# Kernel tuning notes

Measured on AMD Instinct MI355X. Metric: run time of the kernel, lower is better.

Reference implementation:

```python
import jax, jax.numpy as jnp
import numpy as np

ALPHA = 20.0 / 100.0  # dt / tau
NOISE_SCALE = 0.1 * (2.0 * ALPHA) ** 0.5  # network_noise * sqrt(2*alpha)

T, B, I, H, O = 512, 64, 128, 512, 64


def setup_inputs() -> dict:
    key = jax.random.key(0)
    ks = jax.random.split(key, 6)
    s_in = 1.0 / np.sqrt(I)
    s_h = 1.0 / np.sqrt(H)
    return {
        "x": jax.random.normal(ks[0], (T, B, I), jnp.float32),
        "noise": jax.random.normal(ks[1], (T, B, H), jnp.float32),
        "W_in": jax.random.normal(ks[2], (H, I), jnp.float32) * s_in,
        "W_rec": jax.random.normal(ks[3], (H, H), jnp.float32) * s_h,
        "b_rec": jnp.zeros((H,), jnp.float32),
        "W_out": jax.random.normal(ks[4], (O, H), jnp.float32) * s_h,
        "b_out": jnp.zeros((O,), jnp.float32),
    }


def reference(x, noise, W_in, W_rec, b_rec, W_out, b_out):
    # Precompute input projection for all timesteps: (T, B, H)
    xin = jnp.einsum("tbi,hi->tbh", x, W_in)

    def step(hidden, inp):
        xin_t, noise_t = inp
        h_new = jax.nn.relu(xin_t + hidden @ W_rec.T + b_rec)
        h_new = hidden * (1.0 - ALPHA) + h_new * ALPHA
        h_new = h_new + noise_t * NOISE_SCALE
        return h_new, h_new

    h0 = jnp.zeros((x.shape[1], W_rec.shape[0]), x.dtype)
    _, rnn_output = jax.lax.scan(step, h0, (xin, noise))  # (T, B, H)
    output = jnp.einsum("tbh,oh->tbo", rnn_output, W_out) + b_out
    return output, rnn_output
```

## Files before the change

### kernel.cpp

```cpp
#include <hip/hip_runtime.h>

constexpr int T  = 512;
constexpr int NB = 64;
constexpr int NI = 128;
constexpr int NH = 512;
constexpr int NO = 64;

constexpr float ALPHA = 0.2f;
constexpr float NSC   = 0.063245553203367586f;

typedef _Float16 h2_t __attribute__((ext_vector_type(2)));

#if defined(__has_builtin)
#  if __has_builtin(__builtin_amdgcn_fdot2)
#    define HAS_FDOT2 1
#  endif
#endif
#ifndef HAS_FDOT2
#  define HAS_FDOT2 0
#endif

__device__ __forceinline__ float dot2(uint32_t wbits, uint32_t hbits, float acc) {
#if HAS_FDOT2
    return __builtin_amdgcn_fdot2(__builtin_bit_cast(h2_t, wbits),
                                  __builtin_bit_cast(h2_t, hbits), acc, false);
#else
    const h2_t wv = __builtin_bit_cast(h2_t, wbits);
    const h2_t hv = __builtin_bit_cast(h2_t, hbits);
    return acc + (float)wv.x * (float)hv.x + (float)wv.y * (float)hv.y;
#endif
}

__device__ __forceinline__ uint32_t pk2(float x, float y) {
    return __builtin_bit_cast(uint32_t, (h2_t){(_Float16)x, (_Float16)y});
}

__global__ __launch_bounds__(256) void k_gemm_nt_bias(
    const float* __restrict__ A, const float* __restrict__ Bm,
    const float* __restrict__ bias, float* __restrict__ C,
    int M, int N, int K)
{
    __shared__ __align__(16) float As[32][68];
    __shared__ __align__(16) float Bs[32][68];
    const int tid = threadIdx.x;
    const int tx = tid & 15, ty = tid >> 4;
    const long row0 = (long)blockIdx.x * 64;
    const long col0 = (long)blockIdx.y * 64;
    const int lr = tid >> 3;
    const int lq = tid & 7;

    float acc[4][4] = {};

    for (int kt = 0; kt < K; kt += 32) {
        #pragma unroll
        for (int hh = 0; hh < 2; ++hh) {
            const int r = lr + hh * 32;
            const float4 va = *(const float4*)&A[(size_t)(row0 + r) * K + kt + lq * 4];
            As[lq*4+0][r] = va.x; As[lq*4+1][r] = va.y;
            As[lq*4+2][r] = va.z; As[lq*4+3][r] = va.w;
            const float4 vb = *(const float4*)&Bm[(size_t)(col0 + r) * K + kt + lq * 4];
            Bs[lq*4+0][r] = vb.x; Bs[lq*4+1][r] = vb.y;
            Bs[lq*4+2][r] = vb.z; Bs[lq*4+3][r] = vb.w;
        }
        __syncthreads();
        #pragma unroll
        for (int kk = 0; kk < 32; ++kk) {
            const float4 a4 = *(const float4*)&As[kk][ty * 4];
            const float4 b4 = *(const float4*)&Bs[kk][tx * 4];
            const float a[4] = {a4.x, a4.y, a4.z, a4.w};
            const float b[4] = {b4.x, b4.y, b4.z, b4.w};
            #pragma unroll
            for (int i = 0; i < 4; ++i)
                #pragma unroll
                for (int j = 0; j < 4; ++j)
                    acc[i][j] += a[i] * b[j];
        }
        __syncthreads();
    }

    #pragma unroll
    for (int i = 0; i < 4; ++i) {
        const long r = row0 + ty * 4 + i;
        const int  cc = (int)col0 + tx * 4;
        float4 ov;
        ov.x = acc[i][0] + bias[cc + 0];
        ov.y = acc[i][1] + bias[cc + 1];
        ov.z = acc[i][2] + bias[cc + 2];
        ov.w = acc[i][3] + bias[cc + 3];
        *(float4*)&C[(size_t)r * N + cc] = ov;
    }
}

__device__ __forceinline__ uint32_t pack_h(float h, uint32_t tag) {
    const _Float16 hf = (_Float16)h;
    const uint32_t hb = __builtin_bit_cast(unsigned short, hf);
    return (hb << 16) | (tag & 0xFFFFu);
}

__global__ __launch_bounds__(512, 2) void k_rnn(
    const float* __restrict__ W_rec,
    const float* __restrict__ noise,
    float* __restrict__ rnn,
    uint32_t* __restrict__ ex)
{
    const int bid = blockIdx.x;
    const int g = bid & 63;
    const int m = bid >> 6;
    const int tid = threadIdx.x;
    const int w = tid >> 6;
    const int l = tid & 63;

    __shared__ __align__(16) unsigned short hbf[NH];
    __shared__ __align__(16) float pr[8][128];

    uint32_t wa0,wa1,wa2,wa3,wa4,wa5,wa6,wa7,wa8,wa9,wa10,wa11,wa12,wa13,wa14,wa15,
             wa16,wa17,wa18,wa19,wa20,wa21,wa22,wa23,wa24,wa25,wa26,wa27,wa28,wa29,wa30,wa31;
    uint32_t wb0,wb1,wb2,wb3,wb4,wb5,wb6,wb7,wb8,wb9,wb10,wb11,wb12,wb13,wb14,wb15,
             wb16,wb17,wb18,wb19,wb20,wb21,wb22,wb23,wb24,wb25,wb26,wb27,wb28,wb29,wb30,wb31;
    {
        const float* p0 = W_rec + (size_t)(m * 128 + l) * NH + w * 64;
        const float* p1 = W_rec + (size_t)(m * 128 + l + 64) * NH + w * 64;
#define LDW(P, VA, VB, OFF) { const float4 q_ = *(const float4*)((P) + (OFF)); \
                              VA = pk2(q_.x, q_.y); VB = pk2(q_.z, q_.w); }
        LDW(p0, wa0,  wa1,   0) LDW(p0, wa2,  wa3,   4)
        LDW(p0, wa4,  wa5,   8) LDW(p0, wa6,  wa7,  12)
        LDW(p0, wa8,  wa9,  16) LDW(p0, wa10, wa11, 20)
        LDW(p0, wa12, wa13, 24) LDW(p0, wa14, wa15, 28)
        LDW(p0, wa16, wa17, 32) LDW(p0, wa18, wa19, 36)
        LDW(p0, wa20, wa21, 40) LDW(p0, wa22, wa23, 44)
        LDW(p0, wa24, wa25, 48) LDW(p0, wa26, wa27, 52)
        LDW(p0, wa28, wa29, 56) LDW(p0, wa30, wa31, 60)
        LDW(p1, wb0,  wb1,   0) LDW(p1, wb2,  wb3,   4)
        LDW(p1, wb4,  wb5,   8) LDW(p1, wb6,  wb7,  12)
        LDW(p1, wb8,  wb9,  16) LDW(p1, wb10, wb11, 20)
        LDW(p1, wb12, wb13, 24) LDW(p1, wb14, wb15, 28)
        LDW(p1, wb16, wb17, 32) LDW(p1, wb18, wb19, 36)
        LDW(p1, wb20, wb21, 40) LDW(p1, wb22, wb23, 44)
        LDW(p1, wb24, wb25, 48) LDW(p1, wb26, wb27, 52)
        LDW(p1, wb28, wb29, 56) LDW(p1, wb30, wb31, 60)
#undef LDW
    }
#define PIN8(A,B,C,D,E,F,G,H) asm volatile("" : "+v"(A),"+v"(B),"+v"(C),"+v"(D),"+v"(E),"+v"(F),"+v"(G),"+v"(H));
    PIN8(wa0,wa1,wa2,wa3,wa4,wa5,wa6,wa7)
    PIN8(wa8,wa9,wa10,wa11,wa12,wa13,wa14,wa15)
    PIN8(wa16,wa17,wa18,wa19,wa20,wa21,wa22,wa23)
    PIN8(wa24,wa25,wa26,wa27,wa28,wa29,wa30,wa31)
    PIN8(wb0,wb1,wb2,wb3,wb4,wb5,wb6,wb7)
    PIN8(wb8,wb9,wb10,wb11,wb12,wb13,wb14,wb15)
    PIN8(wb16,wb17,wb18,wb19,wb20,wb21,wb22,wb23)
    PIN8(wb24,wb25,wb26,wb27,wb28,wb29,wb30,wb31)
#undef PIN8

    const int gc = m * 128 + tid;

    const int q    = tid - 128;
    const int pp   = q >> 7;
    const int pm   = pp + (pp >= m ? 1 : 0);
    const int pcol = pm * 128 + (q & 127);

    hbf[tid] = 0;

    float hreg = 0.f;

    float xin_pf = 0.f, noi_pf = 0.f;
    if (tid < 128) {
        xin_pf = rnn[(size_t)g * NH + gc];
        noi_pf = noise[(size_t)g * NH + gc];
    }
    __syncthreads();

    int alive  = 1;
    int budget = 1 << 16;

    for (int t = 0; t < T; ++t) {
        float aA0 = 0.f, aA1 = 0.f, aB0 = 0.f, aB1 = 0.f;
        {
            const uint4* hp = (const uint4*)&hbf[w * 64];
#define DOTB(N, A0, A1, A2, A3) { const uint4 u_ = hp[N]; \
            aA0 = dot2(wa##A0, u_.x, aA0); aA1 = dot2(wa##A1, u_.y, aA1); \
            aA0 = dot2(wa##A2, u_.z, aA0); aA1 = dot2(wa##A3, u_.w, aA1); \
            aB0 = dot2(wb##A0, u_.x, aB0); aB1 = dot2(wb##A1, u_.y, aB1); \
            aB0 = dot2(wb##A2, u_.z, aB0); aB1 = dot2(wb##A3, u_.w, aB1); }
            DOTB(0,  0,  1,  2,  3)
            DOTB(1,  4,  5,  6,  7)
            DOTB(2,  8,  9, 10, 11)
            DOTB(3, 12, 13, 14, 15)
            DOTB(4, 16, 17, 18, 19)
            DOTB(5, 20, 21, 22, 23)
            DOTB(6, 24, 25, 26, 27)
            DOTB(7, 28, 29, 30, 31)
#undef DOTB
        }
        pr[w][l]      = aA0 + aA1;
        pr[w][l + 64] = aB0 + aB1;
        __syncthreads();

        const uint32_t want = (uint32_t)(t + 1);
        uint32_t* slot = ex + (size_t)(t & 1) * NB * NH;

        if (tid < 128) {
            float sum = 0.f;
            #pragma unroll
            for (int k = 0; k < 8; ++k) sum += pr[k][tid];
            const float hn = fmaxf(xin_pf + sum, 0.f);
            const float nw = (1.f - ALPHA) * hreg + ALPHA * hn + NSC * noi_pf;
            hreg = nw;
            const uint32_t pk = pack_h(nw, want);
            (void)__hip_atomic_exchange(&slot[(size_t)g * NH + gc], pk,
                                        __ATOMIC_RELAXED, __HIP_MEMORY_SCOPE_AGENT);
            hbf[gc] = (unsigned short)(pk >> 16);
            rnn[((size_t)t * NB + g) * NH + gc] = nw;
            const int tn = (t + 1 < T) ? (t + 1) : t;
            xin_pf = rnn[((size_t)tn * NB + g) * NH + gc];
            noi_pf = noise[((size_t)tn * NB + g) * NH + gc];
        } else {
            uint32_t v;
            if (alive) {
                for (;;) {
                    v = __hip_atomic_fetch_or(&slot[(size_t)g * NH + pcol], 0u,
                                              __ATOMIC_RELAXED, __HIP_MEMORY_SCOPE_AGENT);
                    if ((v & 0xFFFFu) == (want & 0xFFFFu)) break;
                    __builtin_amdgcn_s_sleep(1);
                    if (--budget < 0) { alive = 0; break; }
                }
            } else {
                v = __hip_atomic_fetch_or(&slot[(size_t)g * NH + pcol], 0u,
                                          __ATOMIC_RELAXED, __HIP_MEMORY_SCOPE_AGENT);
            }
            hbf[pcol] = (unsigned short)(v >> 16);
        }
        __syncthreads();
    }
}

extern "C" void kernel_launch(void* const* d_in, const int* in_sizes, int n_in,
                              void* d_out, int out_size, void* d_ws, size_t ws_size,
                              hipStream_t stream)
{
    (void)in_sizes; (void)n_in; (void)out_size; (void)ws_size;
    const float* x     = (const float*)d_in[0];
    const float* noise = (const float*)d_in[1];
    const float* W_in  = (const float*)d_in[2];
    const float* W_rec = (const float*)d_in[3];
    const float* b_rec = (const float*)d_in[4];
    const float* W_out = (const float*)d_in[5];
    const float* b_out = (const float*)d_in[6];

    float* out = (float*)d_out;
    float* rnn = out + (size_t)T * NB * NO;

    uint32_t* ex = (uint32_t*)d_ws;

    hipMemsetAsync(ex, 0, (size_t)2 * NB * NH * sizeof(uint32_t), stream);

    hipLaunchKernelGGL(k_gemm_nt_bias, dim3((T * NB) / 64, NH / 64), dim3(256), 0, stream,
                       x, W_in, b_rec, rnn, T * NB, NH, NI);

    hipLaunchKernelGGL(k_rnn, dim3(256), dim3(512), 0, stream,
                       W_rec, noise, rnn, ex);

    hipLaunchKernelGGL(k_gemm_nt_bias, dim3((T * NB) / 64, NO / 64), dim3(256), 0, stream,
                       rnn, W_out, b_out, out, T * NB, NO, NH);
}
```

Measured before the change: 734.3 us.

## Process two batch rows per RNN block and enlarge GEMM tiles

The recurrent kernel now assigns two batch rows to each workgroup, reusing the register-resident W_rec slice for both. This halves the number of workgroups (128 instead of 256) and the cross-block exchange traffic per row pair, at the cost of double polling and more LDS per block. The projection GEMMs move to templated 128-row tiles with larger per-thread accumulators for better reuse. The inline-asm register pinning of the weights is removed, which may change register allocation.

Result: slower. 1.141 ms (+55.4%).

```diff
diff --git a/kernel.cpp b/kernel.cpp
--- a/kernel.cpp
+++ b/kernel.cpp
@@ -35,59 +35,68 @@
     return __builtin_bit_cast(uint32_t, (h2_t){(_Float16)x, (_Float16)y});
 }
 
-__global__ __launch_bounds__(256) void k_gemm_nt_bias(
+template<int TN>
+__global__ __launch_bounds__(256) void k_gemm_t(
     const float* __restrict__ A, const float* __restrict__ Bm,
     const float* __restrict__ bias, float* __restrict__ C,
     int M, int N, int K)
 {
-    __shared__ __align__(16) float As[32][68];
-    __shared__ __align__(16) float Bs[32][68];
+    constexpr int NA = TN / 16;
+    __shared__ __align__(16) float As[16][132];
+    __shared__ __align__(16) float Bs[16][TN + 4];
     const int tid = threadIdx.x;
     const int tx = tid & 15, ty = tid >> 4;
-    const long row0 = (long)blockIdx.x * 64;
-    const long col0 = (long)blockIdx.y * 64;
-    const int lr = tid >> 3;
-    const int lq = tid & 7;
-
-    float acc[4][4] = {};
-
-    for (int kt = 0; kt < K; kt += 32) {
-        #pragma unroll
-        for (int hh = 0; hh < 2; ++hh) {
-            const int r = lr + hh * 32;
-            const float4 va = *(const float4*)&A[(size_t)(row0 + r) * K + kt + lq * 4];
-            As[lq*4+0][r] = va.x; As[lq*4+1][r] = va.y;
-            As[lq*4+2][r] = va.z; As[lq*4+3][r] = va.w;
-            const float4 vb = *(const float4*)&Bm[(size_t)(col0 + r) * K + kt + lq * 4];
-            Bs[lq*4+0][r] = vb.x; Bs[lq*4+1][r] = vb.y;
-            Bs[lq*4+2][r] = vb.z; Bs[lq*4+3][r] = vb.w;
-        }
-        __syncthreads();
-        #pragma unroll
-        for (int kk = 0; kk < 32; ++kk) {
-            const float4 a4 = *(const float4*)&As[kk][ty * 4];
-            const float4 b4 = *(const float4*)&Bs[kk][tx * 4];
-            const float a[4] = {a4.x, a4.y, a4.z, a4.w};
-            const float b[4] = {b4.x, b4.y, b4.z, b4.w};
+    const long row0 = (long)blockIdx.x * 128;
+    const long col0 = (long)blockIdx.y * TN;
+
+    float acc[8][NA] = {};
+
+    for (int kt = 0; kt < K; kt += 16) {
+        __syncthreads();
+        #pragma unroll
+        for (int f = tid; f < 128 * 4; f += 256) {
+            const int r = f >> 2, ko = (f & 3) * 4;
+            const float4 v = *(const float4*)&A[(row0 + r) * K + kt + ko];
+            As[ko+0][r] = v.x; As[ko+1][r] = v.y;
+            As[ko+2][r] = v.z; As[ko+3][r] = v.w;
+        }
+        #pragma unroll
+        for (int f = tid; f < TN * 4; f += 256) {
+            const int c = f >> 2, ko = (f & 3) * 4;
+            const float4 v = *(const float4*)&Bm[(col0 + c) * K + kt + ko];
+            Bs[ko+0][c] = v.x; Bs[ko+1][c] = v.y;
+            Bs[ko+2][c] = v.z; Bs[ko+3][c] = v.w;
+        }
+        __syncthreads();
+        #pragma unroll
+        for (int kk = 0; kk < 16; ++kk) {
+            float a[8], b[NA];
+            *(float4*)&a[0] = *(const float4*)&As[kk][ty * 8];
+            *(float4*)&a[4] = *(const float4*)&As[kk][ty * 8 + 4];
             #pragma unroll
-            for (int i = 0; i < 4; ++i)
+            for (int j = 0; j < NA; j += 4)
+                *(float4*)&b[j] = *(const float4*)&Bs[kk][tx * NA + j];
+            #pragma unroll
+            for (int i = 0; i < 8; ++i)
                 #pragma unroll
-                for (int j = 0; j < 4; ++j)
+                for (int j = 0; j < NA; ++j)
                     acc[i][j] += a[i] * b[j];
         }
-        __syncthreads();
     }
 
     #pragma unroll
-    for (int i = 0; i < 4; ++i) {
-        const long r = row0 + ty * 4 + i;
-        const int  cc = (int)col0 + tx * 4;
-        float4 ov;
-        ov.x = acc[i][0] + bias[cc + 0];
-        ov.y = acc[i][1] + bias[cc + 1];
-        ov.z = acc[i][2] + bias[cc + 2];
-        ov.w = acc[i][3] + bias[cc + 3];
-        *(float4*)&C[(size_t)r * N + cc] = ov;
+    for (int i = 0; i < 8; ++i) {
+        const long r = row0 + ty * 8 + i;
+        const int cc = (int)col0 + tx * NA;
+        #pragma unroll
+        for (int j = 0; j < NA; j += 4) {
+            float4 ov;
+            ov.x = acc[i][j+0] + bias[cc + j + 0];
+            ov.y = acc[i][j+1] + bias[cc + j + 1];
+            ov.z = acc[i][j+2] + bias[cc + j + 2];
+            ov.w = acc[i][j+3] + bias[cc + j + 3];
+            *(float4*)&C[(size_t)r * N + cc + j] = ov;
+        }
     }
 }
 
@@ -104,14 +113,15 @@
     uint32_t* __restrict__ ex)
 {
     const int bid = blockIdx.x;
-    const int g = bid & 63;
-    const int m = bid >> 6;
+    const int g = bid & 31;
+    const int m = bid >> 5;
     const int tid = threadIdx.x;
     const int w = tid >> 6;
     const int l = tid & 63;
-
-    __shared__ __align__(16) unsigned short hbf[NH];
-    __shared__ __align__(16) float pr[8][128];
+    const int b0 = g * 2, b1 = g * 2 + 1;
+
+    __shared__ __align__(16) unsigned short hbf[2][NH];
+    __shared__ __align__(16) float pr[2][8][128];
 
     uint32_t wa0,wa1,wa2,wa3,wa4,wa5,wa6,wa7,wa8,wa9,wa10,wa11,wa12,wa13,wa14,wa15,
              wa16,wa17,wa18,wa19,wa20,wa21,wa22,wa23,wa24,wa25,wa26,wa27,wa28,wa29,wa30,wa31;
@@ -140,16 +150,6 @@
         LDW(p1, wb28, wb29, 56) LDW(p1, wb30, wb31, 60)
 #undef LDW
     }
-#define PIN8(A,B,C,D,E,F,G,H) asm volatile("" : "+v"(A),"+v"(B),"+v"(C),"+v"(D),"+v"(E),"+v"(F),"+v"(G),"+v"(H));
-    PIN8(wa0,wa1,wa2,wa3,wa4,wa5,wa6,wa7)
-    PIN8(wa8,wa9,wa10,wa11,wa12,wa13,wa14,wa15)
-    PIN8(wa16,wa17,wa18,wa19,wa20,wa21,wa22,wa23)
-    PIN8(wa24,wa25,wa26,wa27,wa28,wa29,wa30,wa31)
-    PIN8(wb0,wb1,wb2,wb3,wb4,wb5,wb6,wb7)
-    PIN8(wb8,wb9,wb10,wb11,wb12,wb13,wb14,wb15)
-    PIN8(wb16,wb17,wb18,wb19,wb20,wb21,wb22,wb23)
-    PIN8(wb24,wb25,wb26,wb27,wb28,wb29,wb30,wb31)
-#undef PIN8
 
     const int gc = m * 128 + tid;
 
@@ -158,14 +158,14 @@
     const int pm   = pp + (pp >= m ? 1 : 0);
     const int pcol = pm * 128 + (q & 127);
 
-    hbf[tid] = 0;
-
-    float hreg = 0.f;
-
-    float xin_pf = 0.f, noi_pf = 0.f;
+    hbf[0][tid] = 0; hbf[1][tid] = 0;
+
+    float hreg0 = 0.f, hreg1 = 0.f;
+
+    float xin0 = 0.f, noi0 = 0.f, xin1 = 0.f, noi1 = 0.f;
     if (tid < 128) {
-        xin_pf = rnn[(size_t)g * NH + gc];
-        noi_pf = noise[(size_t)g * NH + gc];
+        xin0 = rnn[(size_t)b0 * NH + gc];  noi0 = noise[(size_t)b0 * NH + gc];
+        xin1 = rnn[(size_t)b1 * NH + gc];  noi1 = noise[(size_t)b1 * NH + gc];
     }
     __syncthreads();
 
@@ -174,13 +174,19 @@
 
     for (int t = 0; t < T; ++t) {
         float aA0 = 0.f, aA1 = 0.f, aB0 = 0.f, aB1 = 0.f;
+        float cA0 = 0.f, cA1 = 0.f, cB0 = 0.f, cB1 = 0.f;
         {
-            const uint4* hp = (const uint4*)&hbf[w * 64];
-#define DOTB(N, A0, A1, A2, A3) { const uint4 u_ = hp[N]; \
-            aA0 = dot2(wa##A0, u_.x, aA0); aA1 = dot2(wa##A1, u_.y, aA1); \
-            aA0 = dot2(wa##A2, u_.z, aA0); aA1 = dot2(wa##A3, u_.w, aA1); \
-            aB0 = dot2(wb##A0, u_.x, aB0); aB1 = dot2(wb##A1, u_.y, aB1); \
-            aB0 = dot2(wb##A2, u_.z, aB0); aB1 = dot2(wb##A3, u_.w, aB1); }
+            const uint4* hp0 = (const uint4*)&hbf[0][w * 64];
+            const uint4* hp1 = (const uint4*)&hbf[1][w * 64];
+#define DOTB(N, A0, A1, A2, A3) { const uint4 u_ = hp0[N]; const uint4 v_ = hp1[N]; \
+            aA0 = dot2(wa##A0, u_.x, aA0); cA0 = dot2(wa##A0, v_.x, cA0); \
+            aA1 = dot2(wa##A1, u_.y, aA1); cA1 = dot2(wa##A1, v_.y, cA1); \
+            aA0 = dot2(wa##A2, u_.z, aA0); cA0 = dot2(wa##A2, v_.z, cA0); \
+            aA1 = dot2(wa##A3, u_.w, aA1); cA1 = dot2(wa##A3, v_.w, cA1); \
+            aB0 = dot2(wb##A0, u_.x, aB0); cB0 = dot2(wb##A0, v_.x, cB0); \
+            aB1 = dot2(wb##A1, u_.y, aB1); cB1 = dot2(wb##A1, v_.y, cB1); \
+            aB0 = dot2(wb##A2, u_.z, aB0); cB0 = dot2(wb##A2, v_.z, cB0); \
+            aB1 = dot2(wb##A3, u_.w, aB1); cB1 = dot2(wb##A3, v_.w, cB1); }
             DOTB(0,  0,  1,  2,  3)
             DOTB(1,  4,  5,  6,  7)
             DOTB(2,  8,  9, 10, 11)
@@ -191,43 +197,64 @@
             DOTB(7, 28, 29, 30, 31)
 #undef DOTB
         }
-        pr[w][l]      = aA0 + aA1;
-        pr[w][l + 64] = aB0 + aB1;
+        pr[0][w][l]      = aA0 + aA1;
+        pr[0][w][l + 64] = aB0 + aB1;
+        pr[1][w][l]      = cA0 + cA1;
+        pr[1][w][l + 64] = cB0 + cB1;
         __syncthreads();
 
         const uint32_t want = (uint32_t)(t + 1);
         uint32_t* slot = ex + (size_t)(t & 1) * NB * NH;
 
         if (tid < 128) {
-            float sum = 0.f;
+            float s0 = 0.f, s1 = 0.f;
             #pragma unroll
-            for (int k = 0; k < 8; ++k) sum += pr[k][tid];
-            const float hn = fmaxf(xin_pf + sum, 0.f);
-            const float nw = (1.f - ALPHA) * hreg + ALPHA * hn + NSC * noi_pf;
-            hreg = nw;
-            const uint32_t pk = pack_h(nw, want);
-            (void)__hip_atomic_exchange(&slot[(size_t)g * NH + gc], pk,
+            for (int k = 0; k < 8; ++k) { s0 += pr[0][k][tid]; s1 += pr[1][k][tid]; }
+            const float hn0 = fmaxf(xin0 + s0, 0.f);
+            const float hn1 = fmaxf(xin1 + s1, 0.f);
+            const float nw0 = (1.f - ALPHA) * hreg0 + ALPHA * hn0 + NSC * noi0;
+            const float nw1 = (1.f - ALPHA) * hreg1 + ALPHA * hn1 + NSC * noi1;
+            hreg0 = nw0; hreg1 = nw1;
+            const uint32_t pk0 = pack_h(nw0, want);
+            const uint32_t pk1 = pack_h(nw1, want);
+            (void)__hip_atomic_exchange(&slot[(size_t)b0 * NH + gc], pk0,
                                         __ATOMIC_RELAXED, __HIP_MEMORY_SCOPE_AGENT);
-            hbf[gc] = (unsigned short)(pk >> 16);
-            rnn[((size_t)t * NB + g) * NH + gc] = nw;
+            (void)__hip_atomic_exchange(&slot[(size_t)b1 * NH + gc], pk1,
+                                        __ATOMIC_RELAXED, __HIP_MEMORY_SCOPE_AGENT);
+            hbf[0][gc] = (unsigned short)(pk0 >> 16);
+            hbf[1][gc] = (unsigned short)(pk1 >> 16);
+            rnn[((size_t)t * NB + b0) * NH + gc] = nw0;
+            rnn[((size_t)t * NB + b1) * NH + gc] = nw1;
             const int tn = (t + 1 < T) ? (t + 1) : t;
-            xin_pf = rnn[((size_t)tn * NB + g) * NH + gc];
-            noi_pf = noise[((size_t)tn * NB + g) * NH + gc];
+            xin0 = rnn[((size_t)tn * NB + b0) * NH + gc];
+            noi0 = noise[((size_t)tn * NB + b0) * NH + gc];
+            xin1 = rnn[((size_t)tn * NB + b1) * NH + gc];
+            noi1 = noise[((size_t)tn * NB + b1) * NH + gc];
         } else {
-            uint32_t v;
+            uint32_t v0, v1;
             if (alive) {
                 for (;;) {
-                    v = __hip_atomic_fetch_or(&slot[(size_t)g * NH + pcol], 0u,
-                                              __ATOMIC_RELAXED, __HIP_MEMORY_SCOPE_AGENT);
-                    if ((v & 0xFFFFu) == (want & 0xFFFFu)) break;
+                    v0 = __hip_atomic_fetch_or(&slot[(size_t)b0 * NH + pcol], 0u,
+                                               __ATOMIC_RELAXED, __HIP_MEMORY_SCOPE_AGENT);
+                    if ((v0 & 0xFFFFu) == (want & 0xFFFFu)) break;
+                    __builtin_amdgcn_s_sleep(1);
+                    if (--budget < 0) { alive = 0; break; }
+                }
+                for (;;) {
+                    v1 = __hip_atomic_fetch_or(&slot[(size_t)b1 * NH + pcol], 0u,
+                                               __ATOMIC_RELAXED, __HIP_MEMORY_SCOPE_AGENT);
+                    if ((v1 & 0xFFFFu) == (want & 0xFFFFu)) break;
                     __builtin_amdgcn_s_sleep(1);
                     if (--budget < 0) { alive = 0; break; }
                 }
             } else {
-                v = __hip_atomic_fetch_or(&slot[(size_t)g * NH + pcol], 0u,
-                                          __ATOMIC_RELAXED, __HIP_MEMORY_SCOPE_AGENT);
+                v0 = __hip_atomic_fetch_or(&slot[(size_t)b0 * NH + pcol], 0u,
+                                           __ATOMIC_RELAXED, __HIP_MEMORY_SCOPE_AGENT);
+                v1 = __hip_atomic_fetch_or(&slot[(size_t)b1 * NH + pcol], 0u,
+                                           __ATOMIC_RELAXED, __HIP_MEMORY_SCOPE_AGENT);
             }
-            hbf[pcol] = (unsigned short)(v >> 16);
+            hbf[0][pcol] = (unsigned short)(v0 >> 16);
+            hbf[1][pcol] = (unsigned short)(v1 >> 16);
         }
         __syncthreads();
     }
@@ -253,12 +280,12 @@
 
     hipMemsetAsync(ex, 0, (size_t)2 * NB * NH * sizeof(uint32_t), stream);
 
-    hipLaunchKernelGGL(k_gemm_nt_bias, dim3((T * NB) / 64, NH / 64), dim3(256), 0, stream,
-                       x, W_in, b_rec, rnn, T * NB, NH, NI);
-
-    hipLaunchKernelGGL(k_rnn, dim3(256), dim3(512), 0, stream,
+    hipLaunchKernelGGL((k_gemm_t<128>), dim3((T * NB) / 128, NH / 128), dim3(256), 0,
+                       stream, x, W_in, b_rec, rnn, T * NB, NH, NI);
+
+    hipLaunchKernelGGL(k_rnn, dim3(128), dim3(512), 0, stream,
                        W_rec, noise, rnn, ex);
 
-    hipLaunchKernelGGL(k_gemm_nt_bias, dim3((T * NB) / 64, NO / 64), dim3(256), 0, stream,
-                       rnn, W_out, b_out, out, T * NB, NO, NH);
-}
+    hipLaunchKernelGGL((k_gemm_t<64>), dim3((T * NB) / 128, NO / 64), dim3(256), 0,
+                       stream, rnn, W_out, b_out, out, T * NB, NO, NH);
+}
```
